# Optimization experiments

Hardware: AMD Instinct MI355X
Metric: run time of the kernel (lower is better)

## Reference

```python
import jax, jax.numpy as jnp
import numpy as np

B, N, D, H, K, NH = 4096, 2048, 1024, 4096, 5, 8
HD = D // NH  # head dim


def setup_inputs() -> dict:
    key = jax.random.key(0)
    ks = jax.random.split(key, 12)
    s_d = np.float32(1.0 / np.sqrt(D))
    s_h = np.float32(1.0 / np.sqrt(H))
    rn = lambda k, sh, s: jax.random.normal(k, sh, dtype=jnp.float32) * s
    return {
        "morph0": jax.random.normal(ks[0], (B, D), dtype=jnp.float32),
        "stored_morph0": jax.random.normal(ks[1], (N, D), dtype=jnp.float32),
        "stored_morph1": jax.random.normal(ks[2], (N, D), dtype=jnp.float32),
        "wq": rn(ks[3], (D, D), s_d), "bq": jnp.zeros((D,), jnp.float32),
        "wk": rn(ks[4], (D, D), s_d), "bk": jnp.zeros((D,), jnp.float32),
        "wv": rn(ks[5], (D, D), s_d), "bv": jnp.zeros((D,), jnp.float32),
        "wo": rn(ks[6], (D, D), s_d), "bo": jnp.zeros((D,), jnp.float32),
        "w1": rn(ks[7], (H, D), s_d), "b1": jnp.zeros((H,), jnp.float32),
        "w2": rn(ks[8], (H, H), s_h), "b2": jnp.zeros((H,), jnp.float32),
        "w3": rn(ks[9], (D, H), s_h), "b3": jnp.zeros((D,), jnp.float32),
    }


def _l2norm(x):
    # F.normalize(dim=1): x / max(||x||, eps)
    n = jnp.sqrt(jnp.sum(x * x, axis=-1, keepdims=True))
    return x / jnp.maximum(n, 1e-12)


def reference(morph0, stored_morph0, stored_morph1,
              wq, bq, wk, bk, wv, bv, wo, bo,
              w1, b1, w2, b2, w3, b3):
    # ---- retrieve similar patterns: cosine sim + topk + fused gather-subtract ----
    qn = _l2norm(morph0)                       # [B, D]
    sn = _l2norm(stored_morph0)                # [N, D]
    sim = qn @ sn.T                            # [B, N]
    _, top_idx = jax.lax.top_k(sim, K)         # [B, K]
    evo = stored_morph1 - stored_morph0        # [N, D]
    selected = jnp.take(evo, top_idx, axis=0)  # [B, K, D] evolution vectors

    # ---- torch.nn.MultiheadAttention(D, 8, batch_first=True), eval mode ----
    q = (morph0 @ wq.T + bq).reshape(B, 1, NH, HD)      # [B, 1, NH, HD]
    k = (selected @ wk.T + bk).reshape(B, K, NH, HD)    # [B, K, NH, HD]
    v = (selected @ wv.T + bv).reshape(B, K, NH, HD)
    scores = jnp.einsum('bqhd,bkhd->bhqk', q, k) / np.float32(np.sqrt(HD))  # [B, NH, 1, K]
    attn = jax.nn.softmax(scores, axis=-1)
    ctx = jnp.einsum('bhqk,bkhd->bqhd', attn, v).reshape(B, 1, D)
    context = (ctx @ wo.T + bo)[:, 0, :]                # [B, D]
    attn_weights = attn.mean(axis=1)                    # [B, 1, K] (avg over heads)

    # ---- evolution net (dropout inactive in eval) + residual ----
    x = morph0 + context
    h1 = jax.nn.relu(x @ w1.T + b1)
    h2 = jax.nn.relu(h1 @ w2.T + b2)
    predicted = morph0 + (h2 @ w3.T + b3)
    return predicted, attn_weights
```

## Files before the change

### kernel.cpp

```cpp
#include <hip/hip_runtime.h>
#include <hip/hip_bf16.h>
#include <math.h>

typedef __bf16 bf16_t;
typedef __bf16 bf16x4 __attribute__((ext_vector_type(4)));
typedef __bf16 bf16x8 __attribute__((ext_vector_type(8)));
typedef float  f32x4  __attribute__((ext_vector_type(4)));

#define BB 4096
#define NN 2048
#define DD 1024
#define HH 4096
#define KSEL 5
#define NHEAD 8

__device__ __forceinline__ unsigned short bfbits(float f) {
  return __builtin_bit_cast(unsigned short, (bf16_t)f);
}

__device__ __forceinline__ void gload_lds16(const void* g, void* l) {
  __builtin_amdgcn_global_load_lds(
      (const __attribute__((address_space(1))) void*)g,
      (__attribute__((address_space(3))) void*)l, 16, 0, 0);
}

__device__ __forceinline__ ushort4 cvt4(float4 x) {
  ushort4 o;
  o.x = bfbits(x.x); o.y = bfbits(x.y); o.z = bfbits(x.z); o.w = bfbits(x.w);
  return o;
}

#define P_M0   1048576
#define P_S0   1572864
#define P_EVO  2097152
#define P_WQ   2359296
#define P_WKV  2883584
#define P_WO   3145728
#define P_W1   4194304
#define P_W2   8388608
#define P_W3   9437184
#define P_BKV  9437696
__global__ void __launch_bounds__(256)
prep_k(const float4* __restrict__ m0, const float4* __restrict__ s0,
       const float4* __restrict__ s1,
       const float4* __restrict__ wq, const float4* __restrict__ wk,
       const float4* __restrict__ wv, const float4* __restrict__ wo,
       const float4* __restrict__ w1, const float4* __restrict__ w2,
       const float4* __restrict__ w3,
       const float4* __restrict__ bk, const float4* __restrict__ bv,
       ushort4* __restrict__ m0b, ushort4* __restrict__ s0b,
       ushort4* __restrict__ evo,
       ushort4* __restrict__ wqb, ushort4* __restrict__ wkvb,
       ushort4* __restrict__ wob,
       ushort4* __restrict__ w1b, ushort4* __restrict__ w2b,
       ushort4* __restrict__ w3b, float4* __restrict__ bkv)
{
  const int stride = gridDim.x * 256;
  for (int i = blockIdx.x * 256 + threadIdx.x; i < P_BKV; i += stride) {
    if (i < P_M0) {
      m0b[i] = cvt4(m0[i]);
    } else if (i < P_S0) {
      int j = i - P_M0; s0b[j] = cvt4(s0[j]);
    } else if (i < P_EVO) {
      int j = i - P_S0;
      float4 a = s0[j], b = s1[j];
      float4 d; d.x = b.x - a.x; d.y = b.y - a.y; d.z = b.z - a.z; d.w = b.w - a.w;
      evo[j] = cvt4(d);
    } else if (i < P_WQ) {
      int j = i - P_EVO; wqb[j] = cvt4(wq[j]);
    } else if (i < P_WKV) {
      int j = i - P_WQ;
      wkvb[j] = cvt4(j < 262144 ? wk[j] : wv[j - 262144]);
    } else if (i < P_WO) {
      int j = i - P_WKV; wob[j] = cvt4(wo[j]);
    } else if (i < P_W1) {
      int j = i - P_WO; w1b[j] = cvt4(w1[j]);
    } else if (i < P_W2) {
      int j = i - P_W1; w2b[j] = cvt4(w2[j]);
    } else if (i < P_W3) {
      int j = i - P_W2; w3b[j] = cvt4(w3[j]);
    } else {
      int j = i - P_W3;
      bkv[j] = (j < 256) ? bk[j] : bv[j - 256];
    }
  }
}

__global__ void rnormd_k(const float* __restrict__ s0, double* __restrict__ rnd) {
  __shared__ double red[256];
  int n = blockIdx.x, tid = threadIdx.x;
  const float4* row = (const float4*)(s0 + (size_t)n * DD);
  float4 x = row[tid];
  double ss = (double)x.x * x.x + (double)x.y * x.y + (double)x.z * x.z + (double)x.w * x.w;
  red[tid] = ss; __syncthreads();
  for (int s = 128; s > 0; s >>= 1) {
    if (tid < s) red[tid] += red[tid + s];
    __syncthreads();
  }
  if (tid == 0) rnd[n] = 1.0 / fmax(sqrt(red[0]), 1e-12);
}

template<bool RELU, bool RESID, bool OUTBF16>
__global__ void __launch_bounds__(256)
gemm_bt(const bf16_t* __restrict__ A, const bf16_t* __restrict__ Bw,
        const float* __restrict__ bias, const float* __restrict__ resid,
        float* __restrict__ outf, bf16_t* __restrict__ outb,
        int M, int Nn, int Kk)
{
  __shared__ alignas(16) bf16_t At[2][4096];
  __shared__ alignas(16) bf16_t Bt[2][4096];
  const int tid = threadIdx.x;
  const int wave = tid >> 6, lane = tid & 63;
  const int wm = wave >> 1, wn = wave & 1;
  const int bm = blockIdx.y << 7, bn = blockIdx.x << 7;

  const int srow  = (wave << 4) + (lane >> 2);
  const int scolb = (lane & 3) << 4;
  const char* pA0 = (const char*)A  + (size_t)(bm + srow) * Kk * 2 + scolb;
  const char* pA1 = (const char*)A  + (size_t)(bm + srow + 64) * Kk * 2 + scolb;
  const char* pB0 = (const char*)Bw + (size_t)(bn + srow) * Kk * 2 + scolb;
  const char* pB1 = (const char*)Bw + (size_t)(bn + srow + 64) * Kk * 2 + scolb;

  f32x4 zero = {0.f, 0.f, 0.f, 0.f};
  f32x4 acc[4][4];
  #pragma unroll
  for (int i = 0; i < 4; ++i)
    #pragma unroll
    for (int j = 0; j < 4; ++j) acc[i][j] = zero;

  const int fAoff = ((wm << 6) + (lane & 15)) * 32 + ((lane >> 4) << 3);
  const int fBoff = ((wn << 6) + (lane & 15)) * 32 + ((lane >> 4) << 3);

  const int nt = Kk >> 5;
  {
    char* lA = (char*)At[0] + (wave << 10);
    char* lB = (char*)Bt[0] + (wave << 10);
    gload_lds16(pA0, lA);
    gload_lds16(pA1, lA + 4096);
    gload_lds16(pB0, lB);
    gload_lds16(pB1, lB + 4096);
  }
  __syncthreads();

  for (int t = 0; t < nt; ++t) {
    const int cur = t & 1;
    if (t + 1 < nt) {
      size_t kb = (size_t)(t + 1) << 6;
      char* lA = (char*)At[cur ^ 1] + (wave << 10);
      char* lB = (char*)Bt[cur ^ 1] + (wave << 10);
      gload_lds16(pA0 + kb, lA);
      gload_lds16(pA1 + kb, lA + 4096);
      gload_lds16(pB0 + kb, lB);
      gload_lds16(pB1 + kb, lB + 4096);
    }
    bf16x8 av[4], bv[4];
    #pragma unroll
    for (int i = 0; i < 4; ++i) av[i] = *(const bf16x8*)(&At[cur][fAoff + i * 512]);
    #pragma unroll
    for (int j = 0; j < 4; ++j) bv[j] = *(const bf16x8*)(&Bt[cur][fBoff + j * 512]);
    #pragma unroll
    for (int i = 0; i < 4; ++i)
      #pragma unroll
      for (int j = 0; j < 4; ++j)
        acc[i][j] = __builtin_amdgcn_mfma_f32_16x16x32_bf16(av[i], bv[j], acc[i][j], 0, 0, 0);
    __syncthreads();
  }

  const int r0 = bm + (wm << 6) + ((lane >> 4) << 2);
  const int c0 = bn + (wn << 6) + (lane & 15);
  #pragma unroll
  for (int i = 0; i < 4; ++i) {
    #pragma unroll
    for (int j = 0; j < 4; ++j) {
      #pragma unroll
      for (int r = 0; r < 4; ++r) {
        int row = r0 + i * 16 + r;
        int col = c0 + j * 16;
        size_t o = (size_t)row * Nn + col;
        float v = acc[i][j][r];
        if (bias)  v += bias[col];
        if (RESID) v += resid[o];
        if (RELU)  v = fmaxf(v, 0.f);
        if (OUTBF16) outb[o] = (bf16_t)v;
        else         outf[o] = v;
      }
    }
  }
}

template<bool RELU>
__global__ void __launch_bounds__(512, 2)
gemm8p(const bf16_t* __restrict__ A, const bf16_t* __restrict__ Bw,
       const float* __restrict__ bias, bf16_t* __restrict__ outb,
       int Nn, int Kk, int nbx)
{
  __shared__ alignas(16) bf16_t As[2][16384];
  __shared__ alignas(16) bf16_t Bs[2][16384];
  const int tid  = threadIdx.x;
  const int lane = tid & 63, wv = tid >> 6;
  const int wm = wv >> 2, wn = wv & 3;
  const int ln15 = lane & 15, ln4 = lane >> 4;

  const int nwg = gridDim.x;
  const int q = nwg >> 3, r = nwg & 7;
  const int xcd = blockIdx.x & 7, loc = blockIdx.x >> 3;
  const int swz = (xcd < r ? xcd * (q + 1) : r * (q + 1) + (xcd - r) * q) + loc;
  const int bm = (swz / nbx) << 8;
  const int bn = (swz % nbx) << 8;

  const int NT = Kk >> 6;

  f32x4 acc[8][4];
  f32x4 zero = {0.f, 0.f, 0.f, 0.f};
  #pragma unroll
  for (int i = 0; i < 8; ++i)
    #pragma unroll
    for (int j = 0; j < 4; ++j) acc[i][j] = zero;

  auto stageA = [&](int MH, bf16_t* lds, int kt) {
    #pragma unroll
    for (int u = 0; u < 2; ++u) {
      int rowbase = u * 128 + MH * 64 + wv * 8;
      int row = rowbase + (lane >> 3);
      int slot = (lane & 7) ^ (row & 7);
      gload_lds16(A + (size_t)(bm + row) * Kk + kt * 64 + slot * 8,
                  (char*)lds + rowbase * 128);
    }
  };
  auto stageB = [&](int NH, bf16_t* lds, int kt) {
    #pragma unroll
    for (int u = 0; u < 2; ++u) {
      int rowbase = u * 128 + ((wv >> 2) << 6) + NH * 32 + ((wv & 3) << 3);
      int row = rowbase + (lane >> 3);
      int slot = (lane & 7) ^ (row & 7);
      gload_lds16(Bw + (size_t)(bn + row) * Kk + kt * 64 + slot * 8,
                  (char*)lds + rowbase * 128);
    }
  };

  stageA(0, As[0], 0); stageA(1, As[0], 0);
  stageB(0, Bs[0], 0); stageB(1, Bs[0], 0);
  asm volatile("s_waitcnt vmcnt(0)" ::: "memory");
  __builtin_amdgcn_s_barrier();
  __builtin_amdgcn_sched_barrier(0);

#define DS_A(AV, MH, KK)                                                         \
    _Pragma("unroll") for (int mi = 0; mi < 4; ++mi) {                           \
      const int row = wm * 128 + (MH) * 64 + mi * 16 + ln15;                     \
      const int slot = (KK) * 4 + ln4;                                           \
      AV[mi] = *(const bf16x8*)(Ab + row * 128 + ((slot ^ (row & 7)) << 4));     \
    }
#define DS_B(KK)                                                                 \
    _Pragma("unroll") for (int nj = 0; nj < 4; ++nj) {                           \
      const int row = wn * 64 + nj * 16 + ln15;                                  \
      const int slot = (KK) * 4 + ln4;                                           \
      bvv[nj] = *(const bf16x8*)(Bb + row * 128 + ((slot ^ (row & 7)) << 4));    \
    }
#define MMA(AV, MH)                                                              \
    __builtin_amdgcn_s_setprio(1);                                               \
    _Pragma("unroll") for (int mi = 0; mi < 4; ++mi)                             \
      _Pragma("unroll") for (int nj = 0; nj < 4; ++nj)                           \
        acc[(MH)*4+mi][nj] = __builtin_amdgcn_mfma_f32_16x16x32_bf16(            \
            AV[mi], bvv[nj], acc[(MH)*4+mi][nj], 0, 0, 0);                       \
    __builtin_amdgcn_s_setprio(0);

  for (int t = 0; t < NT; ++t) {
    const int cur = t & 1;
    const char* Ab = (const char*)As[cur];
    const char* Bb = (const char*)Bs[cur];
    bf16_t* nA = As[cur ^ 1];
    bf16_t* nB = Bs[cur ^ 1];
    const bool more = (t + 1 < NT);
    bf16x8 ae[4], ao[4], bvv[4];

    DS_A(ae, 0, 0); DS_B(0); DS_A(ao, 1, 0);
    if (more) { stageB(0, nB, t + 1); stageB(1, nB, t + 1); }
    MMA(ae, 0);
    DS_A(ae, 0, 1);
    if (more) { stageA(0, nA, t + 1); stageA(1, nA, t + 1); }
    MMA(ao, 1);
    DS_B(1); DS_A(ao, 1, 1);
    MMA(ae, 0);
    MMA(ao, 1);
    asm volatile("s_waitcnt vmcnt(0)" ::: "memory");
    __builtin_amdgcn_sched_barrier(0);
    __builtin_amdgcn_s_barrier();
    __builtin_amdgcn_sched_barrier(0);
  }
#undef DS_A
#undef DS_B
#undef MMA

  #pragma unroll
  for (int am = 0; am < 8; ++am) {
    #pragma unroll
    for (int an = 0; an < 4; ++an) {
      #pragma unroll
      for (int rr = 0; rr < 4; ++rr) {
        int row = bm + wm * 128 + am * 16 + (lane >> 4) * 4 + rr;
        int col = bn + wn * 64 + an * 16 + ln15;
        float v = acc[am][an][rr] + bias[col];
        if (RELU) v = fmaxf(v, 0.f);
        outb[(size_t)row * Nn + col] = (bf16_t)v;
      }
    }
  }
}

__global__ void __launch_bounds__(256)
topk8_k(const float* __restrict__ sim, const double* __restrict__ rnd,
        int* __restrict__ cand)
{
  __shared__ float vals[NN];
  __shared__ float rv[256];
  __shared__ int   ri[256];
  int b = blockIdx.x, tid = threadIdx.x;
  for (int t = 0; t < NN / 256; ++t) {
    int i = tid + t * 256;
    vals[i] = sim[(size_t)b * NN + i] * (float)rnd[i];
  }
  __syncthreads();
  for (int p = 0; p < 8; ++p) {
    float bvv = -INFINITY; int bi = NN;
    for (int t = 0; t < NN / 256; ++t) {
      int i = tid + t * 256;
      float v = vals[i];
      if (v > bvv) { bvv = v; bi = i; }
    }
    rv[tid] = bvv; ri[tid] = bi;
    __syncthreads();
    for (int s = 128; s > 0; s >>= 1) {
      if (tid < s) {
        float v2 = rv[tid + s]; int i2 = ri[tid + s];
        if (v2 > rv[tid] || (v2 == rv[tid] && i2 < ri[tid])) { rv[tid] = v2; ri[tid] = i2; }
      }
      __syncthreads();
    }
    if (tid == 0) {
      int wsel = ri[0];
      cand[b * 8 + p] = wsel;
      vals[wsel] = -INFINITY;
    }
    __syncthreads();
  }
}

__global__ void __launch_bounds__(256)
refine_k(const float* __restrict__ m0, const float* __restrict__ s0,
         const double* __restrict__ rnd, const int* __restrict__ cand,
         int* __restrict__ topidx)
{
  __shared__ double red[256];
  __shared__ double vals[8];
  int b = blockIdx.x, tid = threadIdx.x;
  int cs[8];
  #pragma unroll
  for (int j = 0; j < 8; ++j) cs[j] = cand[b * 8 + j];
  const float* q = m0 + (size_t)b * DD;
  double part[8];
  #pragma unroll
  for (int j = 0; j < 8; ++j) part[j] = 0.0;
  for (int d = tid; d < DD; d += 256) {
    double qd = (double)q[d];
    #pragma unroll
    for (int j = 0; j < 8; ++j)
      part[j] += qd * (double)s0[(size_t)cs[j] * DD + d];
  }
  for (int j = 0; j < 8; ++j) {
    red[tid] = part[j]; __syncthreads();
    for (int s = 128; s > 0; s >>= 1) {
      if (tid < s) red[tid] += red[tid + s];
      __syncthreads();
    }
    if (tid == 0) vals[j] = red[0] * rnd[cs[j]];
    __syncthreads();
  }
  if (tid == 0) {
    bool used[8] = {false,false,false,false,false,false,false,false};
    for (int p = 0; p < KSEL; ++p) {
      int best = -1;
      for (int j = 0; j < 8; ++j) {
        if (used[j]) continue;
        if (best < 0 || vals[j] > vals[best] ||
            (vals[j] == vals[best] && cs[j] < cs[best])) best = j;
      }
      used[best] = true;
      topidx[b * KSEL + p] = cs[best];
    }
  }
}

__global__ void __launch_bounds__(256)
attn_k(const bf16_t* __restrict__ q, const bf16_t* __restrict__ eKV,
       const int* __restrict__ tidx,
       bf16_t* __restrict__ ctx, float* __restrict__ attn_out)
{
  __shared__ float aw[NHEAD][KSEL];
  const int b = blockIdx.x, t = threadIdx.x;
  const int d0 = t << 2;
  int idx[KSEL];
  #pragma unroll
  for (int j = 0; j < KSEL; ++j) idx[j] = tidx[b * KSEL + j];

  bf16x4 qv = *(const bf16x4*)(q + (size_t)b * DD + d0);
  float s[KSEL];
  #pragma unroll
  for (int j = 0; j < KSEL; ++j) {
    bf16x4 kv = *(const bf16x4*)(eKV + (size_t)idx[j] * 2048 + d0);
    float p = (float)qv[0] * (float)kv[0] + (float)qv[1] * (float)kv[1]
            + (float)qv[2] * (float)kv[2] + (float)qv[3] * (float)kv[3];
    #pragma unroll
    for (int m = 16; m > 0; m >>= 1) p += __shfl_xor(p, m);
    s[j] = p * 0.08838834764831845f;
  }
  float mx = s[0];
  #pragma unroll
  for (int j = 1; j < KSEL; ++j) mx = fmaxf(mx, s[j]);
  float e[KSEL], sum = 0.f;
  #pragma unroll
  for (int j = 0; j < KSEL; ++j) { e[j] = expf(s[j] - mx); sum += e[j]; }
  float inv = 1.f / sum;

  float c0 = 0.f, c1 = 0.f, c2 = 0.f, c3 = 0.f;
  #pragma unroll
  for (int j = 0; j < KSEL; ++j) {
    float a = e[j] * inv;
    bf16x4 vv = *(const bf16x4*)(eKV + (size_t)idx[j] * 2048 + 1024 + d0);
    c0 += a * (float)vv[0]; c1 += a * (float)vv[1];
    c2 += a * (float)vv[2]; c3 += a * (float)vv[3];
    if ((t & 31) == 0) aw[t >> 5][j] = a;
  }
  bf16x4 co; co[0] = (bf16_t)c0; co[1] = (bf16_t)c1; co[2] = (bf16_t)c2; co[3] = (bf16_t)c3;
  *(bf16x4*)(ctx + (size_t)b * DD + d0) = co;
  __syncthreads();
  if (t < KSEL) {
    float m = 0.f;
    #pragma unroll
    for (int hh = 0; hh < NHEAD; ++hh) m += aw[hh][t];
    attn_out[(size_t)b * KSEL + t] = m * 0.125f;
  }
}

extern "C" void kernel_launch(void* const* d_in, const int* in_sizes, int n_in,
                              void* d_out, int out_size, void* d_ws, size_t ws_size,
                              hipStream_t stream) {
  (void)in_sizes; (void)n_in; (void)out_size; (void)ws_size;
  const float* morph0 = (const float*)d_in[0];
  const float* s0     = (const float*)d_in[1];
  const float* s1     = (const float*)d_in[2];
  const float* wq = (const float*)d_in[3];  const float* bq = (const float*)d_in[4];
  const float* wk = (const float*)d_in[5];  const float* bk = (const float*)d_in[6];
  const float* wv = (const float*)d_in[7];  const float* bv = (const float*)d_in[8];
  const float* wo = (const float*)d_in[9];  const float* bo = (const float*)d_in[10];
  const float* w1 = (const float*)d_in[11]; const float* b1 = (const float*)d_in[12];
  const float* w2 = (const float*)d_in[13]; const float* b2 = (const float*)d_in[14];
  const float* w3 = (const float*)d_in[15]; const float* b3 = (const float*)d_in[16];

  char* ws = (char*)d_ws;
  size_t off = 0;
  auto alloc = [&](size_t bytes) { char* p = ws + off; off += (bytes + 255) & ~(size_t)255; return p; };

  float*  sim  = (float*) alloc((size_t)BB * NN * 4);
  bf16_t* m0b  = (bf16_t*)alloc((size_t)BB * DD * 2);
  bf16_t* s0b  = (bf16_t*)alloc((size_t)NN * DD * 2);
  bf16_t* evo  = (bf16_t*)alloc((size_t)NN * DD * 2);
  double* rnd  = (double*)alloc((size_t)NN * 8);
  int*    cand = (int*)   alloc((size_t)BB * 8 * 4);
  int*    tidx = (int*)   alloc((size_t)BB * KSEL * 4);
  bf16_t* qb   = (bf16_t*)alloc((size_t)BB * DD * 2);
  bf16_t* eKVb = (bf16_t*)alloc((size_t)NN * 2048 * 2);
  bf16_t* ctxb = (bf16_t*)alloc((size_t)BB * DD * 2);
  bf16_t* xb   = (bf16_t*)alloc((size_t)BB * DD * 2);
  bf16_t* wqb  = (bf16_t*)alloc((size_t)DD * DD * 2);
  bf16_t* wkvb = (bf16_t*)alloc((size_t)2048 * DD * 2);
  bf16_t* wob  = (bf16_t*)alloc((size_t)DD * DD * 2);
  bf16_t* w1b  = (bf16_t*)alloc((size_t)HH * DD * 2);
  bf16_t* w2b  = (bf16_t*)alloc((size_t)HH * HH * 2);
  bf16_t* w3b  = (bf16_t*)alloc((size_t)DD * HH * 2);
  float*  bkv  = (float*) alloc((size_t)2048 * 4);
  bf16_t* h2b  = (bf16_t*)alloc((size_t)BB * HH * 2);
  bf16_t* h1b  = (bf16_t*)sim;
  float*  attn_out = (float*)d_out + (size_t)BB * DD;

  prep_k<<<dim3(2048), dim3(256), 0, stream>>>(
      (const float4*)morph0, (const float4*)s0, (const float4*)s1,
      (const float4*)wq, (const float4*)wk, (const float4*)wv, (const float4*)wo,
      (const float4*)w1, (const float4*)w2, (const float4*)w3,
      (const float4*)bk, (const float4*)bv,
      (ushort4*)m0b, (ushort4*)s0b, (ushort4*)evo,
      (ushort4*)wqb, (ushort4*)wkvb, (ushort4*)wob,
      (ushort4*)w1b, (ushort4*)w2b, (ushort4*)w3b, (float4*)bkv);
  rnormd_k<<<dim3(NN), dim3(256), 0, stream>>>(s0, rnd);

  gemm_bt<false,false,false><<<dim3(NN/128, BB/128), dim3(256), 0, stream>>>(
      m0b, s0b, nullptr, nullptr, sim, nullptr, BB, NN, DD);
  topk8_k<<<dim3(BB), dim3(256), 0, stream>>>(sim, rnd, cand);
  refine_k<<<dim3(BB), dim3(256), 0, stream>>>(morph0, s0, rnd, cand, tidx);

  gemm_bt<false,false,true><<<dim3(DD/128, BB/128), dim3(256), 0, stream>>>(
      m0b, wqb, bq, nullptr, nullptr, qb, BB, DD, DD);
  gemm_bt<false,false,true><<<dim3(2048/128, NN/128), dim3(256), 0, stream>>>(
      evo, wkvb, bkv, nullptr, nullptr, eKVb, NN, 2048, DD);

  attn_k<<<dim3(BB), dim3(256), 0, stream>>>(qb, eKVb, tidx, ctxb, attn_out);

  gemm_bt<false,true,true><<<dim3(DD/128, BB/128), dim3(256), 0, stream>>>(
      ctxb, wob, bo, morph0, nullptr, xb, BB, DD, DD);

  gemm8p<true><<<dim3((BB/256)*(HH/256)), dim3(512), 0, stream>>>(
      xb, w1b, b1, h1b, HH, DD, HH/256);
  gemm8p<true><<<dim3((BB/256)*(HH/256)), dim3(512), 0, stream>>>(
      h1b, w2b, b2, h2b, HH, HH, HH/256);
  gemm_bt<false,true,false><<<dim3(DD/128, BB/128), dim3(256), 0, stream>>>(
      h2b, w3b, b3, morph0, (float*)d_out, nullptr, BB, DD, HH);
}
```

Baseline: 514.1 us.

## Replace 256x256 BK64 GEMM with smaller 128x256 BK32 tile kernel for MLP layers

Swaps the large-tile gemm8p kernel used for the two hidden MLP GEMMs for a new gemm_hp kernel. It uses 128x256 output tiles, a K step of 32, half the accumulators and much less LDS, with launch bounds raised to 4 blocks per CU. The intent is higher occupancy and more workgroups, so latency is hidden by concurrency rather than the hand-interleaved load/MMA schedule. In exchange, arithmetic intensity per tile drops, there are twice as many barriers per K, and the fine-grained software pipelining is gone.

```diff
diff --git a/kernel.cpp b/kernel.cpp
--- a/kernel.cpp
+++ b/kernel.cpp
@@ -189,13 +189,13 @@
 }
 
 template<bool RELU>
-__global__ void __launch_bounds__(512, 2)
-gemm8p(const bf16_t* __restrict__ A, const bf16_t* __restrict__ Bw,
-       const float* __restrict__ bias, bf16_t* __restrict__ outb,
-       int Nn, int Kk, int nbx)
-{
-  __shared__ alignas(16) bf16_t As[2][16384];
-  __shared__ alignas(16) bf16_t Bs[2][16384];
+__global__ void __launch_bounds__(512, 4)
+gemm_hp(const bf16_t* __restrict__ A, const bf16_t* __restrict__ Bw,
+        const float* __restrict__ bias, bf16_t* __restrict__ outb,
+        int Nn, int Kk, int nbx)
+{
+  __shared__ alignas(16) bf16_t As[2][4096];
+  __shared__ alignas(16) bf16_t Bs[2][8192];
   const int tid  = threadIdx.x;
   const int lane = tid & 63, wv = tid >> 6;
   const int wm = wv >> 2, wn = wv & 3;
@@ -205,99 +205,81 @@
   const int q = nwg >> 3, r = nwg & 7;
   const int xcd = blockIdx.x & 7, loc = blockIdx.x >> 3;
   const int swz = (xcd < r ? xcd * (q + 1) : r * (q + 1) + (xcd - r) * q) + loc;
-  const int bm = (swz / nbx) << 8;
+  const int bm = (swz / nbx) << 7;
   const int bn = (swz % nbx) << 8;
 
-  const int NT = Kk >> 6;
-
-  f32x4 acc[8][4];
+  const int NT = Kk >> 5;
+
+  f32x4 acc[4][4];
   f32x4 zero = {0.f, 0.f, 0.f, 0.f};
   #pragma unroll
-  for (int i = 0; i < 8; ++i)
+  for (int i = 0; i < 4; ++i)
     #pragma unroll
     for (int j = 0; j < 4; ++j) acc[i][j] = zero;
 
-  auto stageA = [&](int MH, bf16_t* lds, int kt) {
+  auto stageA = [&](bf16_t* lds, int kt) {
+    int row = wv * 16 + (lane >> 2);
+    int slot = (lane & 3) ^ (row & 3);
+    gload_lds16(A + (size_t)(bm + row) * Kk + kt * 32 + slot * 8,
+                (char*)lds + wv * 1024);
+  };
+  auto stageB = [&](bf16_t* lds, int kt) {
     #pragma unroll
     for (int u = 0; u < 2; ++u) {
-      int rowbase = u * 128 + MH * 64 + wv * 8;
-      int row = rowbase + (lane >> 3);
-      int slot = (lane & 7) ^ (row & 7);
-      gload_lds16(A + (size_t)(bm + row) * Kk + kt * 64 + slot * 8,
-                  (char*)lds + rowbase * 128);
+      int rowbase = u * 128 + wv * 16;
+      int row = rowbase + (lane >> 2);
+      int slot = (lane & 3) ^ (row & 3);
+      gload_lds16(Bw + (size_t)(bn + row) * Kk + kt * 32 + slot * 8,
+                  (char*)lds + rowbase * 64);
     }
   };
-  auto stageB = [&](int NH, bf16_t* lds, int kt) {
-    #pragma unroll
-    for (int u = 0; u < 2; ++u) {
-      int rowbase = u * 128 + ((wv >> 2) << 6) + NH * 32 + ((wv & 3) << 3);
-      int row = rowbase + (lane >> 3);
-      int slot = (lane & 7) ^ (row & 7);
-      gload_lds16(Bw + (size_t)(bn + row) * Kk + kt * 64 + slot * 8,
-                  (char*)lds + rowbase * 128);
-    }
-  };
-
-  stageA(0, As[0], 0); stageA(1, As[0], 0);
-  stageB(0, Bs[0], 0); stageB(1, Bs[0], 0);
+
+  stageA(As[0], 0); stageB(Bs[0], 0);
   asm volatile("s_waitcnt vmcnt(0)" ::: "memory");
   __builtin_amdgcn_s_barrier();
   __builtin_amdgcn_sched_barrier(0);
-
-#define DS_A(AV, MH, KK)                                                         \
-    _Pragma("unroll") for (int mi = 0; mi < 4; ++mi) {                           \
-      const int row = wm * 128 + (MH) * 64 + mi * 16 + ln15;                     \
-      const int slot = (KK) * 4 + ln4;                                           \
-      AV[mi] = *(const bf16x8*)(Ab + row * 128 + ((slot ^ (row & 7)) << 4));     \
-    }
-#define DS_B(KK)                                                                 \
-    _Pragma("unroll") for (int nj = 0; nj < 4; ++nj) {                           \
-      const int row = wn * 64 + nj * 16 + ln15;                                  \
-      const int slot = (KK) * 4 + ln4;                                           \
-      bvv[nj] = *(const bf16x8*)(Bb + row * 128 + ((slot ^ (row & 7)) << 4));    \
-    }
-#define MMA(AV, MH)                                                              \
-    __builtin_amdgcn_s_setprio(1);                                               \
-    _Pragma("unroll") for (int mi = 0; mi < 4; ++mi)                             \
-      _Pragma("unroll") for (int nj = 0; nj < 4; ++nj)                           \
-        acc[(MH)*4+mi][nj] = __builtin_amdgcn_mfma_f32_16x16x32_bf16(            \
-            AV[mi], bvv[nj], acc[(MH)*4+mi][nj], 0, 0, 0);                       \
-    __builtin_amdgcn_s_setprio(0);
 
   for (int t = 0; t < NT; ++t) {
     const int cur = t & 1;
     const char* Ab = (const char*)As[cur];
     const char* Bb = (const char*)Bs[cur];
-    bf16_t* nA = As[cur ^ 1];
-    bf16_t* nB = Bs[cur ^ 1];
     const bool more = (t + 1 < NT);
-    bf16x8 ae[4], ao[4], bvv[4];
-
-    DS_A(ae, 0, 0); DS_B(0); DS_A(ao, 1, 0);
-    if (more) { stageB(0, nB, t + 1); stageB(1, nB, t + 1); }
-    MMA(ae, 0);
-    DS_A(ae, 0, 1);
-    if (more) { stageA(0, nA, t + 1); stageA(1, nA, t + 1); }
-    MMA(ao, 1);
-    DS_B(1); DS_A(ao, 1, 1);
-    MMA(ae, 0);
-    MMA(ao, 1);
+    bf16x8 av[4], bv[4];
+
+    #pragma unroll
+    for (int mi = 0; mi < 4; ++mi) {
+      const int row = wm * 64 + mi * 16 + ln15;
+      av[mi] = *(const bf16x8*)(Ab + row * 64 + ((ln4 ^ (row & 3)) << 4));
+    }
+    #pragma unroll
+    for (int nj = 0; nj < 4; ++nj) {
+      const int row = wn * 64 + nj * 16 + ln15;
+      bv[nj] = *(const bf16x8*)(Bb + row * 64 + ((ln4 ^ (row & 3)) << 4));
+    }
+    if (more) { stageA(As[cur ^ 1], t + 1); stageB(Bs[cur ^ 1], t + 1); }
+
+    __builtin_amdgcn_s_setprio(1);
+    #pragma unroll
+    for (int mi = 0; mi < 4; ++mi)
+      #pragma unroll
+      for (int nj = 0; nj < 4; ++nj)
+        acc[mi][nj] = __builtin_amdgcn_mfma_f32_16x16x32_bf16(
+            av[mi], bv[nj], acc[mi][nj], 0, 0, 0);
+    __builtin_amdgcn_s_setprio(0);
+
     asm volatile("s_waitcnt vmcnt(0)" ::: "memory");
     __builtin_amdgcn_sched_barrier(0);
     __builtin_amdgcn_s_barrier();
     __builtin_amdgcn_sched_barrier(0);
   }
-#undef DS_A
-#undef DS_B
-#undef MMA
-
-  #pragma unroll
-  for (int am = 0; am < 8; ++am) {
+
+  #pragma unroll
+  for (int am = 0; am < 4; ++am) {
     #pragma unroll
     for (int an = 0; an < 4; ++an) {
       #pragma unroll
       for (int rr = 0; rr < 4; ++rr) {
-        int row = bm + wm * 128 + am * 16 + (lane >> 4) * 4 + rr;
+        int row = bm + wm * 64 + am * 16 + (lane >> 4) * 4 + rr;
         int col = bn + wn * 64 + an * 16 + ln15;
         float v = acc[am][an][rr] + bias[col];
         if (RELU) v = fmaxf(v, 0.f);
@@ -507,9 +489,9 @@
   gemm_bt<false,true,true><<<dim3(DD/128, BB/128), dim3(256), 0, stream>>>(
       ctxb, wob, bo, morph0, nullptr, xb, BB, DD, DD);
 
-  gemm8p<true><<<dim3((BB/256)*(HH/256)), dim3(512), 0, stream>>>(
+  gemm_hp<true><<<dim3((BB/128)*(HH/256)), dim3(512), 0, stream>>>(
       xb, w1b, b1, h1b, HH, DD, HH/256);
-  gemm8p<true><<<dim3((BB/256)*(HH/256)), dim3(512), 0, stream>>>(
+  gemm_hp<true><<<dim3((BB/128)*(HH/256)), dim3(512), 0, stream>>>(
       h1b, w2b, b2, h2b, HH, HH, HH/256);
   gemm_bt<false,true,false><<<dim3(DD/128, BB/128), dim3(256), 0, stream>>>(
       h2b, w3b, b3, morph0, (float*)d_out, nullptr, BB, DD, HH);
```

Result: slower. 534.4 us (+4.0%).
